# Kernel tuning notes

Hardware: AMD Instinct MI355X
Metric: run time of the kernel (lower is better)

The kernel has to match this reference:

```python
import jax, jax.numpy as jnp
import numpy as np

B = 524288      # batch
CONT = 64       # continuous features
N_CATE = 16     # categorical fields
VOCAB = 1000    # vocab per field
EM = 8          # embedding dim
LOW = EM * N_CATE + CONT  # 192
R = 32          # representation dim
RH = 32         # rep hidden dim
PH = 16         # head hidden dim
N_HEAD = 8      # number of routing heads


def setup_inputs() -> dict:
    key = jax.random.key(0)
    ks = jax.random.split(key, 16)
    s = 0.05
    return {
        "x_cont": jax.random.normal(ks[0], (B, CONT), dtype=jnp.float32),
        "x_cate": jax.random.randint(ks[1], (B, N_CATE), 0, VOCAB, dtype=jnp.int64),
        "t": jax.random.randint(ks[2], (B, 1), 0, N_HEAD, dtype=jnp.int64),
        # embedding tables, one per categorical field
        "emb": jax.random.normal(ks[3], (N_CATE, VOCAB, EM), dtype=jnp.float32) * s,
        # representation DNN: LOW -> RH -> RH -> R (2 hidden layers + output)
        "W1": jax.random.normal(ks[4], (LOW, RH), dtype=jnp.float32) * s,
        "b1": jnp.zeros((RH,), dtype=jnp.float32),
        "W2": jax.random.normal(ks[5], (RH, RH), dtype=jnp.float32) * s,
        "b2": jnp.zeros((RH,), dtype=jnp.float32),
        "W3": jax.random.normal(ks[6], (RH, R), dtype=jnp.float32) * s,
        "b3": jnp.zeros((R,), dtype=jnp.float32),
        # stacked per-head DNNs: R -> PH -> 1 (1 hidden layer + output)
        "HW1": jax.random.normal(ks[7], (N_HEAD, R, PH), dtype=jnp.float32) * s,
        "Hb1": jnp.zeros((N_HEAD, PH), dtype=jnp.float32),
        "HW2": jax.random.normal(ks[8], (N_HEAD, PH, 1), dtype=jnp.float32) * s,
        "Hb2": jnp.zeros((N_HEAD, 1), dtype=jnp.float32),
    }


def reference(x_cont, x_cate, t, emb, W1, b1, W2, b2, W3, b3, HW1, Hb1, HW2, Hb2):
    # LowFeature: embed each categorical field and concat with continuous
    # emb[f, x_cate[:, f]] -> [B, N_CATE, EM]
    e = emb[jnp.arange(N_CATE)[None, :], x_cate]
    x = jnp.concatenate([x_cont, e.reshape(e.shape[0], -1)], axis=1)  # [B, LOW]
    # representation DNN (eval mode: dropout is identity)
    h = jax.nn.relu(x @ W1 + b1)
    h = jax.nn.relu(h @ W2 + b2)
    r = h @ W3 + b3  # [B, R]
    # evaluate all heads batched, then gather the routed head per sample
    hh = jax.nn.relu(jnp.einsum('br,nrh->bnh', r, HW1) + Hb1[None])  # [B, N_HEAD, PH]
    y_all = jnp.einsum('bnh,nho->bno', hh, HW2) + Hb2[None]          # [B, N_HEAD, 1]
    y = jnp.take_along_axis(y_all[..., 0], t, axis=1)[:, 0]          # [B]
    return y
```

## Files before the change

kernel.cpp:

```cpp
#include <hip/hip_runtime.h>

namespace {

typedef float  f32x4  __attribute__((ext_vector_type(4)));
typedef float  f32x16 __attribute__((ext_vector_type(16)));
typedef short  bf16x8 __attribute__((ext_vector_type(8)));
typedef int    i32x4  __attribute__((ext_vector_type(4)));
typedef unsigned int u32;

constexpr int kRows  = 524288;
constexpr int kCont  = 64;
constexpr int kNCate = 16;
constexpr int kVocab = 1000;
constexpr int kEm    = 8;
constexpr int kRH    = 32;
constexpr int kPH    = 16;

constexpr int    kNFrag = 48;
constexpr size_t kOffEH = (size_t)kNFrag * 1024;

__device__ inline u32 rne_hi(float x) {
    u32 u = __float_as_uint(x);
    return ((u + 0x7fffu + ((u >> 16) & 1u)) >> 16) & 0xffffu;
}
__device__ inline float hi_f32(u32 h) { return __uint_as_float(h << 16); }
__device__ inline u32 pack2(float a, float b) {
    return rne_hi(a) | (rne_hi(b) << 16);
}

union FragU { u32 w[4]; bf16x8 v; uint4 u4; };

__device__ inline f32x16 mfma16(bf16x8 a, bf16x8 b, f32x16 c) {
    return __builtin_amdgcn_mfma_f32_32x32x16_bf16(a, b, c, 0, 0, 0);
}
__device__ inline f32x16 zero16() {
    f32x16 z;
#pragma unroll
    for (int i = 0; i < 16; ++i) z[i] = 0.f;
    return z;
}
__device__ inline void gload_lds16(const void* g, void* l) {
    __builtin_amdgcn_global_load_lds(
        (const __attribute__((address_space(1))) void*)g,
        (__attribute__((address_space(3))) void*)l, 16, 0, 0);
}
__device__ inline void fence_vm0() {
    asm volatile("s_waitcnt vmcnt(0)" ::: "memory");
    __builtin_amdgcn_sched_barrier(0);
}
__device__ inline void fence_lgkm0() {
    asm volatile("s_waitcnt lgkmcnt(0)" ::: "memory");
    __builtin_amdgcn_sched_barrier(0);
}

__global__ __launch_bounds__(256) void build_wfrags(
    const float* __restrict__ W1, const float* __restrict__ W2,
    const float* __restrict__ W3, const float* __restrict__ HW1,
    ushort* __restrict__ WF)
{
    int gid = blockIdx.x * blockDim.x + threadIdx.x;
    if (gid >= kNFrag * 64) return;
    const int q = gid >> 6, l = gid & 63;
    const int lc = l & 31, g = l >> 5;

    const float* src; int k0, col, ldn, p;
    if (q < 12) {
        src = W1; col = lc; ldn = 32; p = 0;
        k0 = (q < 4) ? (16*q + 8*g) : (64 + 8*(q - 4) + 64*g);
    } else if (q < 24) {
        int f = q - 12;
        src = W1; col = lc; ldn = 32; p = 1;
        k0 = (f < 4) ? (16*f + 8*g) : (64 + 8*(f - 4) + 64*g);
    }
    else if (q < 28) { int u2 = q-24; src = W2; k0 = 16*(u2>>1) + 8*g; col = lc; ldn = 32; p = u2&1; }
    else if (q < 32) { int u2 = q-28; src = W3; k0 = 16*(u2>>1) + 8*g; col = lc; ldn = 32; p = u2&1; }
    else {
        int u2 = q-32; int n = u2>>2; int f = (u2>>1)&1; p = u2&1;
        int c128 = n*32 + lc; int head = c128 >> 4, ph = c128 & 15;
        src = HW1 + (size_t)head * kRH * kPH + ph;
        k0 = 16*f + 8*g; col = 0; ldn = kPH;
    }

    u32 hv[8];
#pragma unroll
    for (int j = 0; j < 8; ++j) {
        float w = src[(size_t)(k0 + j) * ldn + col];
        u32 h = rne_hi(w);
        hv[j] = (p == 0) ? h : rne_hi(w - hi_f32(h));
    }
    FragU fu;
#pragma unroll
    for (int w = 0; w < 4; ++w) fu.w[w] = hv[2*w] | (hv[2*w+1] << 16);
    ((uint4*)WF)[q * 64 + l] = fu.u4;
}

__global__ __launch_bounds__(256) void build_embhi(
    const float* __restrict__ emb, ushort* __restrict__ eh)
{
    int r = blockIdx.x * blockDim.x + threadIdx.x;
    if (r >= kNCate * kVocab) return;
    const float* e = emb + (size_t)r * kEm;
    FragU H;
#pragma unroll
    for (int w = 0; w < 4; ++w)
        H.w[w] = pack2(e[2*w], e[2*w+1]);
    ((uint4*)eh)[r] = H.u4;
}

__device__ inline void transition(const float* v, int g, FragU* H, FragU* L) {
    u32 hw[8], lw[8];
#pragma unroll
    for (int p = 0; p < 8; ++p) {
        float v0 = v[2*p], v1 = v[2*p+1];
        u32 h0 = rne_hi(v0), h1 = rne_hi(v1);
        hw[p] = h0 | (h1 << 16);
        lw[p] = pack2(v0 - hi_f32(h0), v1 - hi_f32(h1));
    }
#pragma unroll
    for (int f2 = 0; f2 < 2; ++f2) {
        u32 hp[4], lp[4];
#pragma unroll
        for (int p = 0; p < 4; ++p) {
            hp[p] = (u32)__shfl_xor((int)hw[4*f2 + p], 32);
            lp[p] = (u32)__shfl_xor((int)lw[4*f2 + p], 32);
        }
        H[f2].w[0] = g ? hp[2] : hw[4*f2+0];
        H[f2].w[1] = g ? hp[3] : hw[4*f2+1];
        H[f2].w[2] = g ? hw[4*f2+2] : hp[0];
        H[f2].w[3] = g ? hw[4*f2+3] : hp[1];
        L[f2].w[0] = g ? lp[2] : lw[4*f2+0];
        L[f2].w[1] = g ? lp[3] : lw[4*f2+1];
        L[f2].w[2] = g ? lw[4*f2+2] : lp[0];
        L[f2].w[3] = g ? lw[4*f2+3] : lp[1];
    }
}

__global__ __launch_bounds__(256, 3) void fused_main(
    const float* __restrict__ xc, const int* __restrict__ xcate,
    const int* __restrict__ tptr,
    const ushort* __restrict__ WF,
    const ushort* __restrict__ eh,
    const float* __restrict__ b1, const float* __restrict__ b2,
    const float* __restrict__ b3, const float* __restrict__ Hb1,
    const float* __restrict__ HW2, const float* __restrict__ Hb2,
    float* __restrict__ out)
{
    __shared__ __align__(16) uint4 sW4[16 * 64];
    __shared__ __align__(16) float sX[4][2048];
    __shared__ __align__(16) float sB[360];

    const int tid = threadIdx.x;
    const uint4* wf4 = (const uint4*)WF;

#pragma unroll
    for (int it = 0; it < 4; ++it) {
        const int i = tid + 256 * it;
        sW4[i] = wf4[i];
    }
    for (int i = tid; i < 360; i += 256) {
        float v;
        if      (i < 32)  v = b1[i];
        else if (i < 64)  v = b2[i - 32];
        else if (i < 96)  v = b3[i - 64];
        else if (i < 224) v = Hb1[i - 96];
        else if (i < 352) v = HW2[i - 224];
        else              v = Hb2[i - 352];
        sB[i] = v;
    }
    __syncthreads();

    const int wv = tid >> 6, l = tid & 63;
    const int lc = l & 31, g = l >> 5;
    const int rowbase = blockIdx.x * 256 + wv * 64;
    char* xb = (char*)&sX[wv][0];
    const uint4* eh4 = (const uint4*)eh;

    auto stage_x = [&](int tbase) {
        const float* xbase = xc + (size_t)tbase * kCont;
#pragma unroll
        for (int i = 0; i < 8; ++i) {
            const int r   = 4*i + (l >> 4);
            const int c4s = (l & 15) ^ (r & 15);
            gload_lds16(xbase + r * kCont + c4s * 4, xb + i * 1024);
        }
    };
    auto load_idx = [&](int tbase, i32x4* iq, int& t_lane) {
        const i32x4* cr4 = (const i32x4*)(xcate + (size_t)(tbase + lc) * kNCate + 8*g);
        iq[0] = cr4[0];
        iq[1] = cr4[1];
        t_lane = tptr[tbase + lc];
    };
    auto gather_emb = [&](const i32x4* iq, uint4* ehv) {
#pragma unroll
        for (int i = 0; i < 8; ++i) {
            const int c   = i + 8*g;
            const int idx = (i < 4) ? iq[0][i] : iq[1][i - 4];
            ehv[i] = eh4[(size_t)(c * kVocab + idx)];
        }
    };
    auto layer1_cont = [&](f32x16& acca, f32x16& accb) {
#pragma unroll
        for (int f = 0; f < 4; ++f) {
            const int c0 = 4*f + 2*g;
            f32x4 va0 = *(const f32x4*)(xb + lc*256 + (((c0)     ^ (lc & 15)) * 16));
            f32x4 va1 = *(const f32x4*)(xb + lc*256 + (((c0 + 1) ^ (lc & 15)) * 16));
            FragU H, L;
#pragma unroll
            for (int w = 0; w < 4; ++w) {
                const f32x4& va = (w < 2) ? va0 : va1;
                const float v0 = va[2*(w & 1)], v1 = va[2*(w & 1) + 1];
                u32 h0 = rne_hi(v0), h1 = rne_hi(v1);
                H.w[w] = h0 | (h1 << 16);
                L.w[w] = pack2(v0 - hi_f32(h0), v1 - hi_f32(h1));
            }
            FragU WH, WL;
            WH.u4 = sW4[f * 64 + l];
            WL.u4 = sW4[(12 + f) * 64 + l];
            f32x16& acc = (f & 1) ? accb : acca;
            acc = mfma16(WH.v, H.v, acc);
            acc = mfma16(WL.v, H.v, acc);
            acc = mfma16(WH.v, L.v, acc);
        }
    };
    auto layer1_emb = [&](const uint4* ehv, f32x16& acca, f32x16& accb) {
#pragma unroll
        for (int i = 0; i < 8; ++i) {
            const int f = 4 + i;
            FragU BH, WH;
            BH.u4 = ehv[i];
            WH.u4 = sW4[f * 64 + l];
            f32x16& acc = (f & 1) ? accb : acca;
            acc = mfma16(WH.v, BH.v, acc);
        }
    };
    auto mid = [&](const f32x16& acca, const f32x16& accb, FragU* a4h, FragU* a4l) {
        float v1v[16];
#pragma unroll
        for (int p = 0; p < 4; ++p) {
            f32x4 bq = *(const f32x4*)&sB[0 + 8*p + 4*g];
#pragma unroll
            for (int m = 0; m < 4; ++m)
                v1v[4*p + m] = fmaxf(acca[4*p + m] + accb[4*p + m] + bq[m], 0.f);
        }
        FragU a2h[2], a2l[2];
        transition(v1v, g, a2h, a2l);

        f32x16 acc2 = zero16();
#pragma unroll
        for (int f2 = 0; f2 < 2; ++f2) {
            FragU WH, WL;
            WH.u4 = wf4[(24 + 2*f2) * 64 + l];
            WL.u4 = wf4[(25 + 2*f2) * 64 + l];
            acc2 = mfma16(WH.v, a2h[f2].v, acc2);
            acc2 = mfma16(WL.v, a2h[f2].v, acc2);
            acc2 = mfma16(WH.v, a2l[f2].v, acc2);
        }
        float v2v[16];
#pragma unroll
        for (int p = 0; p < 4; ++p) {
            f32x4 bq = *(const f32x4*)&sB[32 + 8*p + 4*g];
#pragma unroll
            for (int m = 0; m < 4; ++m)
                v2v[4*p + m] = fmaxf(acc2[4*p + m] + bq[m], 0.f);
        }
        FragU a3h[2], a3l[2];
        transition(v2v, g, a3h, a3l);

        f32x16 acc3 = zero16();
#pragma unroll
        for (int f2 = 0; f2 < 2; ++f2) {
            FragU WH, WL;
            WH.u4 = wf4[(28 + 2*f2) * 64 + l];
            WL.u4 = wf4[(29 + 2*f2) * 64 + l];
            acc3 = mfma16(WH.v, a3h[f2].v, acc3);
            acc3 = mfma16(WL.v, a3h[f2].v, acc3);
            acc3 = mfma16(WH.v, a3l[f2].v, acc3);
        }
        float v3v[16];
#pragma unroll
        for (int p = 0; p < 4; ++p) {
            f32x4 bq = *(const f32x4*)&sB[64 + 8*p + 4*g];
#pragma unroll
            for (int m = 0; m < 4; ++m)
                v3v[4*p + m] = acc3[4*p + m] + bq[m];
        }
        transition(v3v, g, a4h, a4l);
    };
    auto heads_store = [&](const FragU* a4h, const FragU* a4l, int t_lane, int arow) {
        const f32x4 hb1q0 = *(const f32x4*)&sB[96  + t_lane*16 + 4*g];
        const f32x4 hb1q1 = *(const f32x4*)&sB[96  + t_lane*16 + 8 + 4*g];
        const f32x4 hw2q0 = *(const f32x4*)&sB[224 + t_lane*16 + 4*g];
        const f32x4 hw2q1 = *(const f32x4*)&sB[224 + t_lane*16 + 8 + 4*g];

        float ys = 0.f;
#pragma unroll
        for (int n = 0; n < 4; ++n) {
            f32x16 hacc = zero16();
#pragma unroll
            for (int f2 = 0; f2 < 2; ++f2) {
                FragU WH, WL;
                WH.u4 = wf4[(32 + 4*n + 2*f2) * 64 + l];
                WL.u4 = wf4[(33 + 4*n + 2*f2) * 64 + l];
                hacc = mfma16(WH.v, a4h[f2].v, hacc);
                hacc = mfma16(WL.v, a4h[f2].v, hacc);
                hacc = mfma16(WH.v, a4l[f2].v, hacc);
            }
            const bool sel = ((t_lane >> 1) == n);
            const bool half = (t_lane & 1);
#pragma unroll
            for (int j = 0; j < 8; ++j) {
                const float bb = (j < 4) ? hb1q0[j] : hb1q1[j - 4];
                const float ww = (j < 4) ? hw2q0[j] : hw2q1[j - 4];
                const float c0 = fmaxf(hacc[j]     + bb, 0.f) * ww;
                const float c1 = fmaxf(hacc[8 + j] + bb, 0.f) * ww;
                const float pick = half ? c1 : c0;
                ys += sel ? pick : 0.f;
            }
        }
        const float ytot = ys + __shfl_xor(ys, 32);
        if (g == 0)
            out[arow] = ytot + sB[352 + t_lane];
    };

    const int tb1 = rowbase, tb2 = rowbase + 32;

    stage_x(tb1);
    i32x4 iq1[2]; int t1;
    load_idx(tb1, iq1, t1);

    fence_vm0();

    uint4 ehv1[8];
    gather_emb(iq1, ehv1);

    f32x16 acca = zero16(), accb = zero16();
    layer1_cont(acca, accb);

    fence_lgkm0();
    stage_x(tb2);
    i32x4 iq2[2]; int t2;
    load_idx(tb2, iq2, t2);

    layer1_emb(ehv1, acca, accb);
    FragU a4h[2], a4l[2];
    mid(acca, accb, a4h, a4l);

    uint4 ehv2[8];
    gather_emb(iq2, ehv2);

    heads_store(a4h, a4l, t1, tb1 + lc);

    fence_vm0();

    acca = zero16(); accb = zero16();
    layer1_cont(acca, accb);
    layer1_emb(ehv2, acca, accb);
    mid(acca, accb, a4h, a4l);
    heads_store(a4h, a4l, t2, tb2 + lc);
}

}

extern "C" void kernel_launch(void* const* d_in, const int* in_sizes, int n_in,
                              void* d_out, int out_size, void* d_ws, size_t ws_size,
                              hipStream_t stream)
{
    const float* x_cont = (const float*)d_in[0];
    const int*   x_cate = (const int*)  d_in[1];
    const int*   t      = (const int*)  d_in[2];
    const float* emb    = (const float*)d_in[3];
    const float* W1     = (const float*)d_in[4];
    const float* b1     = (const float*)d_in[5];
    const float* W2     = (const float*)d_in[6];
    const float* b2     = (const float*)d_in[7];
    const float* W3     = (const float*)d_in[8];
    const float* b3     = (const float*)d_in[9];
    const float* HW1    = (const float*)d_in[10];
    const float* Hb1    = (const float*)d_in[11];
    const float* HW2    = (const float*)d_in[12];
    const float* Hb2    = (const float*)d_in[13];
    float* out = (float*)d_out;

    ushort* WF = (ushort*)d_ws;
    ushort* eh = (ushort*)((char*)d_ws + kOffEH);

    hipLaunchKernelGGL(build_wfrags, dim3(12), dim3(256), 0, stream, W1, W2, W3, HW1, WF);
    hipLaunchKernelGGL(build_embhi, dim3((kNCate*kVocab + 255)/256), dim3(256), 0, stream,
                       emb, eh);

    const int grid = kRows / 256;
    hipLaunchKernelGGL(fused_main, dim3(grid), dim3(256), 0, stream,
                       x_cont, x_cate, t, WF, eh,
                       b1, b2, b3, Hb1, HW2, Hb2, out);
}
```

Before: 74.98 us.

## Fold W3 and b3 into per-head first-layer weights to drop a matmul layer

Because the representation output layer has no nonlinearity, W3·HW1 and b3·HW1+Hb1 are precomputed in a small setup kernel. The main kernel then feeds the second hidden layer's activations straight into the head matmuls, skipping the third layer's MFMAs, its bias add and one bf16 split/transition per tile. This costs an extra tiny kernel launch, and it changes rounding slightly because the fused weights are built in fp32 and then split into hi/lo bf16.

```diff
diff --git a/kernel.cpp b/kernel.cpp
--- a/kernel.cpp
+++ b/kernel.cpp
@@ -18,6 +18,8 @@
 
 constexpr int    kNFrag = 48;
 constexpr size_t kOffEH = (size_t)kNFrag * 1024;
+constexpr size_t kOffHG = kOffEH + 256000;
+constexpr size_t kOffHB = kOffHG + 16384;
 
 __device__ inline u32 rne_hi(float x) {
     u32 u = __float_as_uint(x);
@@ -53,9 +55,34 @@
     __builtin_amdgcn_sched_barrier(0);
 }
 
+__global__ __launch_bounds__(256) void build_hg(
+    const float* __restrict__ W3, const float* __restrict__ HW1,
+    const float* __restrict__ b3, const float* __restrict__ Hb1,
+    float* __restrict__ HG, float* __restrict__ Hb1p)
+{
+    const int gid = blockIdx.x * blockDim.x + threadIdx.x;
+    if (gid < 8 * 32 * 16) {
+        const int n = gid >> 9, k = (gid >> 4) & 31, ph = gid & 15;
+        const float* w3r = W3 + k * 32;
+        const float* h1p = HW1 + (size_t)n * kRH * kPH + ph;
+        float s = 0.f;
+#pragma unroll
+        for (int j = 0; j < 32; ++j) s = fmaf(w3r[j], h1p[j * kPH], s);
+        HG[gid] = s;
+    }
+    if (gid < 128) {
+        const int n = gid >> 4, ph = gid & 15;
+        const float* h1p = HW1 + (size_t)n * kRH * kPH + ph;
+        float s = Hb1[n * kPH + ph];
+#pragma unroll
+        for (int j = 0; j < 32; ++j) s = fmaf(b3[j], h1p[j * kPH], s);
+        Hb1p[gid] = s;
+    }
+}
+
 __global__ __launch_bounds__(256) void build_wfrags(
     const float* __restrict__ W1, const float* __restrict__ W2,
-    const float* __restrict__ W3, const float* __restrict__ HW1,
+    const float* __restrict__ W3, const float* __restrict__ HG,
     ushort* __restrict__ WF)
 {
     int gid = blockIdx.x * blockDim.x + threadIdx.x;
@@ -77,7 +104,7 @@
     else {
         int u2 = q-32; int n = u2>>2; int f = (u2>>1)&1; p = u2&1;
         int c128 = n*32 + lc; int head = c128 >> 4, ph = c128 & 15;
-        src = HW1 + (size_t)head * kRH * kPH + ph;
+        src = HG + (size_t)head * kRH * kPH + ph;
         k0 = 16*f + 8*g; col = 0; ldn = kPH;
     }
 
@@ -141,13 +168,13 @@
     const ushort* __restrict__ WF,
     const ushort* __restrict__ eh,
     const float* __restrict__ b1, const float* __restrict__ b2,
-    const float* __restrict__ b3, const float* __restrict__ Hb1,
+    const float* __restrict__ Hb1p,
     const float* __restrict__ HW2, const float* __restrict__ Hb2,
     float* __restrict__ out)
 {
     __shared__ __align__(16) uint4 sW4[16 * 64];
     __shared__ __align__(16) float sX[4][2048];
-    __shared__ __align__(16) float sB[360];
+    __shared__ __align__(16) float sB[328];
 
     const int tid = threadIdx.x;
     const uint4* wf4 = (const uint4*)WF;
@@ -157,14 +184,13 @@
         const int i = tid + 256 * it;
         sW4[i] = wf4[i];
     }
-    for (int i = tid; i < 360; i += 256) {
+    for (int i = tid; i < 328; i += 256) {
         float v;
         if      (i < 32)  v = b1[i];
         else if (i < 64)  v = b2[i - 32];
-        else if (i < 96)  v = b3[i - 64];
-        else if (i < 224) v = Hb1[i - 96];
-        else if (i < 352) v = HW2[i - 224];
-        else              v = Hb2[i - 352];
+        else if (i < 192) v = Hb1p[i - 64];
+        else if (i < 320) v = HW2[i - 192];
+        else              v = Hb2[i - 320];
         sB[i] = v;
     }
     __syncthreads();
@@ -233,7 +259,7 @@
             acc = mfma16(WH.v, BH.v, acc);
         }
     };
-    auto mid = [&](const f32x16& acca, const f32x16& accb, FragU* a4h, FragU* a4l) {
+    auto mid = [&](const f32x16& acca, const f32x16& accb, FragU* aHh, FragU* aHl) {
         float v1v[16];
 #pragma unroll
         for (int p = 0; p < 4; ++p) {
@@ -263,34 +289,13 @@
             for (int m = 0; m < 4; ++m)
                 v2v[4*p + m] = fmaxf(acc2[4*p + m] + bq[m], 0.f);
         }
-        FragU a3h[2], a3l[2];
-        transition(v2v, g, a3h, a3l);
-
-        f32x16 acc3 = zero16();
-#pragma unroll
-        for (int f2 = 0; f2 < 2; ++f2) {
-            FragU WH, WL;
-            WH.u4 = wf4[(28 + 2*f2) * 64 + l];
-            WL.u4 = wf4[(29 + 2*f2) * 64 + l];
-            acc3 = mfma16(WH.v, a3h[f2].v, acc3);
-            acc3 = mfma16(WL.v, a3h[f2].v, acc3);
-            acc3 = mfma16(WH.v, a3l[f2].v, acc3);
-        }
-        float v3v[16];
-#pragma unroll
-        for (int p = 0; p < 4; ++p) {
-            f32x4 bq = *(const f32x4*)&sB[64 + 8*p + 4*g];
-#pragma unroll
-            for (int m = 0; m < 4; ++m)
-                v3v[4*p + m] = acc3[4*p + m] + bq[m];
-        }
-        transition(v3v, g, a4h, a4l);
-    };
-    auto heads_store = [&](const FragU* a4h, const FragU* a4l, int t_lane, int arow) {
-        const f32x4 hb1q0 = *(const f32x4*)&sB[96  + t_lane*16 + 4*g];
-        const f32x4 hb1q1 = *(const f32x4*)&sB[96  + t_lane*16 + 8 + 4*g];
-        const f32x4 hw2q0 = *(const f32x4*)&sB[224 + t_lane*16 + 4*g];
-        const f32x4 hw2q1 = *(const f32x4*)&sB[224 + t_lane*16 + 8 + 4*g];
+        transition(v2v, g, aHh, aHl);
+    };
+    auto heads_store = [&](const FragU* aHh, const FragU* aHl, int t_lane, int arow) {
+        const f32x4 hb1q0 = *(const f32x4*)&sB[64  + t_lane*16 + 4*g];
+        const f32x4 hb1q1 = *(const f32x4*)&sB[64  + t_lane*16 + 8 + 4*g];
+        const f32x4 hw2q0 = *(const f32x4*)&sB[192 + t_lane*16 + 4*g];
+        const f32x4 hw2q1 = *(const f32x4*)&sB[192 + t_lane*16 + 8 + 4*g];
 
         float ys = 0.f;
 #pragma unroll
@@ -301,9 +306,9 @@
                 FragU WH, WL;
                 WH.u4 = wf4[(32 + 4*n + 2*f2) * 64 + l];
                 WL.u4 = wf4[(33 + 4*n + 2*f2) * 64 + l];
-                hacc = mfma16(WH.v, a4h[f2].v, hacc);
-                hacc = mfma16(WL.v, a4h[f2].v, hacc);
-                hacc = mfma16(WH.v, a4l[f2].v, hacc);
+                hacc = mfma16(WH.v, aHh[f2].v, hacc);
+                hacc = mfma16(WL.v, aHh[f2].v, hacc);
+                hacc = mfma16(WH.v, aHl[f2].v, hacc);
             }
             const bool sel = ((t_lane >> 1) == n);
             const bool half = (t_lane & 1);
@@ -319,7 +324,7 @@
         }
         const float ytot = ys + __shfl_xor(ys, 32);
         if (g == 0)
-            out[arow] = ytot + sB[352 + t_lane];
+            out[arow] = ytot + sB[320 + t_lane];
     };
 
     const int tb1 = rowbase, tb2 = rowbase + 32;
@@ -342,21 +347,21 @@
     load_idx(tb2, iq2, t2);
 
     layer1_emb(ehv1, acca, accb);
-    FragU a4h[2], a4l[2];
-    mid(acca, accb, a4h, a4l);
+    FragU aHh[2], aHl[2];
+    mid(acca, accb, aHh, aHl);
 
     uint4 ehv2[8];
     gather_emb(iq2, ehv2);
 
-    heads_store(a4h, a4l, t1, tb1 + lc);
+    heads_store(aHh, aHl, t1, tb1 + lc);
 
     fence_vm0();
 
     acca = zero16(); accb = zero16();
     layer1_cont(acca, accb);
     layer1_emb(ehv2, acca, accb);
-    mid(acca, accb, a4h, a4l);
-    heads_store(a4h, a4l, t2, tb2 + lc);
+    mid(acca, accb, aHh, aHl);
+    heads_store(aHh, aHl, t2, tb2 + lc);
 }
 
 }
@@ -381,15 +386,20 @@
     const float* Hb2    = (const float*)d_in[13];
     float* out = (float*)d_out;
 
-    ushort* WF = (ushort*)d_ws;
-    ushort* eh = (ushort*)((char*)d_ws + kOffEH);
-
-    hipLaunchKernelGGL(build_wfrags, dim3(12), dim3(256), 0, stream, W1, W2, W3, HW1, WF);
+    ushort* WF   = (ushort*)d_ws;
+    ushort* eh   = (ushort*)((char*)d_ws + kOffEH);
+    float*  HG   = (float*) ((char*)d_ws + kOffHG);
+    float*  Hb1p = (float*) ((char*)d_ws + kOffHB);
+
+    hipLaunchKernelGGL(build_hg, dim3(16), dim3(256), 0, stream,
+                       W3, HW1, b3, Hb1, HG, Hb1p);
+    hipLaunchKernelGGL(build_wfrags, dim3(12), dim3(256), 0, stream,
+                       W1, W2, W3, HG, WF);
     hipLaunchKernelGGL(build_embhi, dim3((kNCate*kVocab + 255)/256), dim3(256), 0, stream,
                        emb, eh);
 
     const int grid = kRows / 256;
     hipLaunchKernelGGL(fused_main, dim3(grid), dim3(256), 0, stream,
                        x_cont, x_cate, t, WF, eh,
-                       b1, b2, b3, Hb1, HW2, Hb2, out);
-}
+                       b1, b2, Hb1p, HW2, Hb2, out);
+}
```

Result: no change. 75.20 us (+0.3%).
